# Kernel optimization log

Hardware: AMD Instinct MI355X
Metric: run time of the kernel (lower is better)

The kernel has to match this reference:

```python
import jax, jax.numpy as jnp
import numpy as np

BLOCK_SIZE = 1024
OUTLIER_SIGMA = 3.0
OUT_FEATURES = 11008
IN_FEATURES = 4096
TOKENS = 64


def _quantize_mixed_np(W):
    """Faithful numpy port of quantize_mixed (BLOCK_SIZE divides numel exactly here)."""
    flat = W.astype(np.float32).reshape(-1)
    nb = flat.size // BLOCK_SIZE
    blocks = flat.reshape(nb, BLOCK_SIZE)
    mu = blocks.mean(axis=1, keepdims=True)
    sig = np.maximum(blocks.std(axis=1, ddof=1, keepdims=True), 1e-8)  # torch.std is unbiased
    outlier = np.abs(blocks - mu) > OUTLIER_SIGMA * sig
    abs_max = np.maximum(np.abs(np.where(outlier, 0.0, blocks)).max(axis=1), 1e-8)
    scales = (abs_max / 127.0).astype(np.float16)
    q = np.clip(np.round(blocks / abs_max[:, None] * 127.0), -127, 127).astype(np.int8)
    all_pos = np.arange(nb, dtype=np.int64)[:, None] * BLOCK_SIZE + np.arange(BLOCK_SIZE, dtype=np.int64)[None, :]
    int8_data = q[~outlier]                      # row-major == torch order
    fp16_data = blocks[outlier].astype(np.float16)
    int8_pos = all_pos[~outlier].astype(np.int32)
    fp16_pos = all_pos[outlier].astype(np.int32)
    block_idx = np.nonzero(~outlier)[0].astype(np.int32)  # block index per int8 value
    return int8_data, fp16_data, scales, int8_pos, fp16_pos, block_idx


def setup_inputs() -> dict:
    key = jax.random.key(0)
    k_x, k_b = jax.random.split(key)
    rng = np.random.default_rng(0)
    W = (rng.standard_normal((OUT_FEATURES, IN_FEATURES)) * 0.02).astype(np.float32)
    int8_data, fp16_data, scales, int8_pos, fp16_pos, block_idx = _quantize_mixed_np(W)
    x = jax.random.normal(k_x, (TOKENS, IN_FEATURES), dtype=jnp.float16)
    bias = jax.random.normal(k_b, (OUT_FEATURES,), dtype=jnp.float16) * jnp.float16(0.02)
    return {
        "x": x,
        "int8_data": jnp.asarray(int8_data),
        "fp16_data": jnp.asarray(fp16_data),
        "scales": jnp.asarray(scales),
        "bias": bias,
        "int8_pos": jnp.asarray(int8_pos),
        "fp16_pos": jnp.asarray(fp16_pos),
        "block_idx": jnp.asarray(block_idx),
    }


def reference(x, int8_data, fp16_data, scales, bias, int8_pos, fp16_pos, block_idx):
    out_features = bias.shape[0]
    in_features = x.shape[1]
    numel = out_features * in_features  # divisible by BLOCK_SIZE for these dims
    # dequantize_mixed: scatter fp16 outliers and dequantized int8 values into flat fp16 buffer
    flat = jnp.zeros((numel,), dtype=jnp.float16)
    flat = flat.at[fp16_pos].set(fp16_data)
    flat = flat.at[int8_pos].set(int8_data.astype(jnp.float16) * scales[block_idx])
    W = flat.reshape(out_features, in_features)
    # F.linear(x, W, bias) in fp16
    return jnp.dot(x.astype(jnp.float16), W.T) + bias
```

## Files before the change

### kernel.cpp

```cpp
#include <hip/hip_runtime.h>
#include <hip/hip_fp16.h>

#define TOK   64
#define INF   4096
#define OUTF  11008
#define NSLC  (OUTF * INF / 64)
#define NBLK  (OUTF / 16)
#define KSPL  4

typedef __attribute__((ext_vector_type(8))) _Float16 half8;
typedef __attribute__((ext_vector_type(4))) _Float16 half4;
typedef __attribute__((ext_vector_type(4))) float floatx4;

__global__ __launch_bounds__(256) void precompute_kernel(
    const float* __restrict__ x, const int* __restrict__ fppos, int nf,
    _Float16* __restrict__ x16, int* __restrict__ cum64) {
  const int t = blockIdx.x * 256 + threadIdx.x;
  if (t < (TOK * INF) / 4) {
    const floatx4 f = *(const floatx4*)&x[t * 4];
    half4 h;
    h[0] = (_Float16)f[0]; h[1] = (_Float16)f[1];
    h[2] = (_Float16)f[2]; h[3] = (_Float16)f[3];
    *(half4*)&x16[t * 4] = h;
  }
  if (t <= NSLC) {
    const int target = t << 6;
    int lo = 0, hi = nf;
    while (lo < hi) {
      const int mid = (lo + hi) >> 1;
      if (fppos[mid] < target) lo = mid + 1; else hi = mid;
    }
    cum64[t] = lo;
  }
}

__global__ __launch_bounds__(256) void fused_gemm_kernel(
    const _Float16* __restrict__ x16, const int* __restrict__ i8,
    const float* __restrict__ fpdat, const int* __restrict__ fppos,
    const float* __restrict__ scales, const float* __restrict__ bias,
    const int* __restrict__ cum64, float* __restrict__ out, int n8) {
  __shared__ float red[4 * 64 * 16];

  const int tid  = threadIdx.x;
  const int wave = tid >> 6;
  const int lane = tid & 63;
  const int quad = lane >> 4;
  const int ln   = lane & 15;
  const int nt   = blockIdx.x >> 2;
  const int kq   = blockIdx.x & 3;
  const int n0   = nt * 16;

  const int r  = n0 + ln;
  const float s = scales[r * 4 + kq];
  const int kb = kq * 1024 + wave * 256 + quad * 8;
  const int pbase = r * INF + kb;

  const _Float16* ap = &x16[ln * INF + kb];

  floatx4 acc0 = {0,0,0,0}, acc1 = {0,0,0,0}, acc2 = {0,0,0,0}, acc3 = {0,0,0,0};

  int c0a[8], c1a[8];
#pragma unroll
  for (int st = 0; st < 8; ++st) {
    const int sI = (pbase + st * 32) >> 6;
    c0a[st] = cum64[sI];
    c1a[st] = cum64[sI + 1];
  }

#pragma unroll
  for (int st = 0; st < 8; ++st) {
    const int p  = pbase + st * 32;
    const int c0 = c0a[st], c1 = c1a[st];

    int f = 0, lt = 0;
    for (int j = c0; j < c1; ++j) {
      const int d = fppos[j] - p;
      lt += (d < 0);
      f |= ((unsigned)d < 8u) ? (1 << d) : 0;
    }

    const int i0 = p - c0 - lt;
    half8 bh;
    if ((f == 0) & (i0 + 8 <= n8)) {
      int l[8];
      __builtin_memcpy(l, &i8[i0], 32);
#pragma unroll
      for (int e = 0; e < 8; ++e) bh[e] = (_Float16)((float)l[e] * s);
    } else {
      int q = i0, jo = c0 + lt;
      const int m = n8 - 1;
#pragma unroll
      for (int e = 0; e < 8; ++e) {
        const int flg = (f >> e) & 1;
        float v;
        if (flg) { v = fpdat[jo]; ++jo; }
        else     { v = (float)i8[q > m ? m : q] * s; ++q; }
        bh[e] = (_Float16)v;
      }
    }

    const int ko = st * 32;
    const half8 a0 = *(const half8*)&ap[ko];
    const half8 a1 = *(const half8*)&ap[16 * INF + ko];
    const half8 a2 = *(const half8*)&ap[32 * INF + ko];
    const half8 a3 = *(const half8*)&ap[48 * INF + ko];
    acc0 = __builtin_amdgcn_mfma_f32_16x16x32_f16(a0, bh, acc0, 0, 0, 0);
    acc1 = __builtin_amdgcn_mfma_f32_16x16x32_f16(a1, bh, acc1, 0, 0, 0);
    acc2 = __builtin_amdgcn_mfma_f32_16x16x32_f16(a2, bh, acc2, 0, 0, 0);
    acc3 = __builtin_amdgcn_mfma_f32_16x16x32_f16(a3, bh, acc3, 0, 0, 0);
  }

  const int mb = quad * 4;
#pragma unroll
  for (int i = 0; i < 4; ++i) red[wave * 1024 + (mb + i)      * 16 + ln] = acc0[i];
#pragma unroll
  for (int i = 0; i < 4; ++i) red[wave * 1024 + (16 + mb + i) * 16 + ln] = acc1[i];
#pragma unroll
  for (int i = 0; i < 4; ++i) red[wave * 1024 + (32 + mb + i) * 16 + ln] = acc2[i];
#pragma unroll
  for (int i = 0; i < 4; ++i) red[wave * 1024 + (48 + mb + i) * 16 + ln] = acc3[i];
  __syncthreads();

#pragma unroll
  for (int c2 = 0; c2 < 4; ++c2) {
    const int cell = tid + c2 * 256;
    const int mm = cell >> 4, nn = cell & 15;
    float v = red[cell] + red[1024 + cell] + red[2048 + cell] + red[3072 + cell];
    if (kq == 0) v += bias[n0 + nn];
    atomicAdd(&out[mm * OUTF + n0 + nn], v);
  }
}

extern "C" void kernel_launch(void* const* d_in, const int* in_sizes, int n_in,
                              void* d_out, int out_size, void* d_ws,
                              size_t ws_size, hipStream_t stream) {
  const float* x      = (const float*)d_in[0];
  const int*   i8     = (const int*)d_in[1];
  const float* fpdat  = (const float*)d_in[2];
  const float* scales = (const float*)d_in[3];
  const float* bias   = (const float*)d_in[4];
  const int*   fppos  = (const int*)d_in[6];

  char* wsp = (char*)d_ws;
  _Float16* x16   = (_Float16*)wsp;
  int*      cum64 = (int*)(wsp + (size_t)TOK * INF * sizeof(_Float16));
  float*    out   = (float*)d_out;

  const int n8 = in_sizes[1];
  const int nf = in_sizes[2];

  hipMemsetAsync(out, 0, (size_t)out_size * sizeof(float), stream);
  precompute_kernel<<<(NSLC + 256) / 256 + 1, 256, 0, stream>>>(x, fppos, nf,
                                                                x16, cum64);
  fused_gemm_kernel<<<NBLK * KSPL, 256, 0, stream>>>(x16, i8, fpdat, fppos,
                                                     scales, bias, cum64, out,
                                                     n8);
}
```

Measured before the change: 488.9 us.

## Dequantize weight block into shared memory with coalesced int8 loads

The precompute step now builds a prefix-sum of outlier counts per 1024-element quantization block rather than per 64-element slice, which makes the precompute grid much smaller. The GEMM kernel first loads each row's outliers into shared memory. It then streams the int8 values for the whole block with coalesced vector loads, places each dequantized value at its shifted position in a padded shared-memory tile, and runs the MFMA loop from LDS. This replaces the per-thread scans over fppos and the scattered gathers inside the MFMA loop. The trade-offs are a per-element linear scan over up to 24 outlier keys, serial outlier handling by one thread per row, and outliers beyond 24 per block are silently dropped.

Result: no change. 486.5 us (-0.5%).

```diff
diff --git a/kernel.cpp b/kernel.cpp
--- a/kernel.cpp
+++ b/kernel.cpp
@@ -4,9 +4,11 @@
 #define TOK   64
 #define INF   4096
 #define OUTF  11008
-#define NSLC  (OUTF * INF / 64)
+#define NQB   44032
 #define NBLK  (OUTF / 16)
 #define KSPL  4
+#define BPAD  1032
+#define MAXO  24
 
 typedef __attribute__((ext_vector_type(8))) _Float16 half8;
 typedef __attribute__((ext_vector_type(4))) _Float16 half4;
@@ -14,7 +16,7 @@
 
 __global__ __launch_bounds__(256) void precompute_kernel(
     const float* __restrict__ x, const int* __restrict__ fppos, int nf,
-    _Float16* __restrict__ x16, int* __restrict__ cum64) {
+    _Float16* __restrict__ x16, int* __restrict__ cum) {
   const int t = blockIdx.x * 256 + threadIdx.x;
   if (t < (TOK * INF) / 4) {
     const floatx4 f = *(const floatx4*)&x[t * 4];
@@ -23,83 +25,110 @@
     h[2] = (_Float16)f[2]; h[3] = (_Float16)f[3];
     *(half4*)&x16[t * 4] = h;
   }
-  if (t <= NSLC) {
-    const int target = t << 6;
+  if (t <= NQB) {
+    const int target = t << 10;
     int lo = 0, hi = nf;
     while (lo < hi) {
       const int mid = (lo + hi) >> 1;
       if (fppos[mid] < target) lo = mid + 1; else hi = mid;
     }
-    cum64[t] = lo;
+    cum[t] = lo;
   }
 }
 
-__global__ __launch_bounds__(256) void fused_gemm_kernel(
+__global__ __launch_bounds__(256) void fused_kernel(
     const _Float16* __restrict__ x16, const int* __restrict__ i8,
     const float* __restrict__ fpdat, const int* __restrict__ fppos,
     const float* __restrict__ scales, const float* __restrict__ bias,
-    const int* __restrict__ cum64, float* __restrict__ out, int n8) {
-  __shared__ float red[4 * 64 * 16];
+    const int* __restrict__ cum, float* __restrict__ out, int n8) {
+  __shared__ __align__(16) _Float16 Bs[16 * BPAD];
+  __shared__ int   key_sh[16][MAXO];
+  __shared__ float oval_sh[16][MAXO];
 
-  const int tid  = threadIdx.x;
+  const int tid = threadIdx.x;
+  const int nt  = blockIdx.x >> 2;
+  const int kq  = blockIdx.x & 3;
+  const int n0  = nt * 16;
+
+  const int rr = tid >> 4;
+  const int jj = tid & 15;
+  const int r  = n0 + rr;
+  const int b  = r * 4 + kq;
+  const int T0 = cum[b], T1 = cum[b + 1];
+  const int nbout = T1 - T0;
+  const int nbo   = nbout < MAXO ? nbout : MAXO;
+  const int pos0  = r * INF + kq * 1024;
+  const int c_lo  = pos0 - T0;
+  const int nint  = 1024 - nbout;
+  const float s   = scales[b];
+
+  if (jj == 0) {
+    for (int i = 0; i < nbo; ++i) {
+      const int o = fppos[T0 + i] - pos0;
+      key_sh[rr][i] = o - i;
+      oval_sh[rr][i] = fpdat[T0 + i];
+    }
+  }
+  __syncthreads();
+
+  const int off  = c_lo & 3;
+  const int c_al = c_lo - off;
+#pragma unroll
+  for (int it = 0; it < 16; ++it) {
+    const int gi = c_al + 4 * (jj + 16 * it);
+    const int t0 = 4 * (jj + 16 * it) - off;
+    int l[4];
+    if (gi + 3 < n8) {
+      __builtin_memcpy(l, &i8[gi], 16);
+    } else {
+#pragma unroll
+      for (int e = 0; e < 4; ++e) {
+        int idx = gi + e; if (idx > n8 - 1) idx = n8 - 1;
+        l[e] = i8[idx];
+      }
+    }
+#pragma unroll
+    for (int e = 0; e < 4; ++e) {
+      const int t = t0 + e;
+      if ((unsigned)t < (unsigned)nint) {
+        int sft = 0;
+        for (int i = 0; i < nbo; ++i) sft += (key_sh[rr][i] <= t);
+        Bs[rr * BPAD + t + sft] = (_Float16)((float)l[e] * s);
+      }
+    }
+  }
+  if (off != 0 && jj == 0) {
+#pragma unroll
+    for (int e = 0; e < 4; ++e) {
+      const int t = 1024 - off + e;
+      if ((unsigned)t < (unsigned)nint) {
+        int idx = c_al + 1024 + e; if (idx > n8 - 1) idx = n8 - 1;
+        int sft = 0;
+        for (int i = 0; i < nbo; ++i) sft += (key_sh[rr][i] <= t);
+        Bs[rr * BPAD + t + sft] = (_Float16)((float)i8[idx] * s);
+      }
+    }
+  }
+  if (jj == 0) {
+    for (int i = 0; i < nbo; ++i)
+      Bs[rr * BPAD + key_sh[rr][i] + i] = (_Float16)oval_sh[rr][i];
+  }
+  __syncthreads();
+
   const int wave = tid >> 6;
   const int lane = tid & 63;
   const int quad = lane >> 4;
   const int ln   = lane & 15;
-  const int nt   = blockIdx.x >> 2;
-  const int kq   = blockIdx.x & 3;
-  const int n0   = nt * 16;
-
-  const int r  = n0 + ln;
-  const float s = scales[r * 4 + kq];
-  const int kb = kq * 1024 + wave * 256 + quad * 8;
-  const int pbase = r * INF + kb;
+  const int kb   = kq * 1024 + wave * 256 + quad * 8;
 
   const _Float16* ap = &x16[ln * INF + kb];
+  const _Float16* bp = &Bs[ln * BPAD + wave * 256 + quad * 8];
 
   floatx4 acc0 = {0,0,0,0}, acc1 = {0,0,0,0}, acc2 = {0,0,0,0}, acc3 = {0,0,0,0};
-
-  int c0a[8], c1a[8];
 #pragma unroll
   for (int st = 0; st < 8; ++st) {
-    const int sI = (pbase + st * 32) >> 6;
-    c0a[st] = cum64[sI];
-    c1a[st] = cum64[sI + 1];
-  }
-
-#pragma unroll
-  for (int st = 0; st < 8; ++st) {
-    const int p  = pbase + st * 32;
-    const int c0 = c0a[st], c1 = c1a[st];
-
-    int f = 0, lt = 0;
-    for (int j = c0; j < c1; ++j) {
-      const int d = fppos[j] - p;
-      lt += (d < 0);
-      f |= ((unsigned)d < 8u) ? (1 << d) : 0;
-    }
-
-    const int i0 = p - c0 - lt;
-    half8 bh;
-    if ((f == 0) & (i0 + 8 <= n8)) {
-      int l[8];
-      __builtin_memcpy(l, &i8[i0], 32);
-#pragma unroll
-      for (int e = 0; e < 8; ++e) bh[e] = (_Float16)((float)l[e] * s);
-    } else {
-      int q = i0, jo = c0 + lt;
-      const int m = n8 - 1;
-#pragma unroll
-      for (int e = 0; e < 8; ++e) {
-        const int flg = (f >> e) & 1;
-        float v;
-        if (flg) { v = fpdat[jo]; ++jo; }
-        else     { v = (float)i8[q > m ? m : q] * s; ++q; }
-        bh[e] = (_Float16)v;
-      }
-    }
-
     const int ko = st * 32;
+    const half8 bh = *(const half8*)&bp[ko];
     const half8 a0 = *(const half8*)&ap[ko];
     const half8 a1 = *(const half8*)&ap[16 * INF + ko];
     const half8 a2 = *(const half8*)&ap[32 * INF + ko];
@@ -109,7 +138,9 @@
     acc2 = __builtin_amdgcn_mfma_f32_16x16x32_f16(a2, bh, acc2, 0, 0, 0);
     acc3 = __builtin_amdgcn_mfma_f32_16x16x32_f16(a3, bh, acc3, 0, 0, 0);
   }
+  __syncthreads();
 
+  float* red = (float*)Bs;
   const int mb = quad * 4;
 #pragma unroll
   for (int i = 0; i < 4; ++i) red[wave * 1024 + (mb + i)      * 16 + ln] = acc0[i];
@@ -142,17 +173,15 @@
   const int*   fppos  = (const int*)d_in[6];
 
   char* wsp = (char*)d_ws;
-  _Float16* x16   = (_Float16*)wsp;
-  int*      cum64 = (int*)(wsp + (size_t)TOK * INF * sizeof(_Float16));
-  float*    out   = (float*)d_out;
+  _Float16* x16 = (_Float16*)wsp;
+  int*      cum = (int*)(wsp + (size_t)TOK * INF * sizeof(_Float16));
+  float*    out = (float*)d_out;
 
   const int n8 = in_sizes[1];
   const int nf = in_sizes[2];
 
   hipMemsetAsync(out, 0, (size_t)out_size * sizeof(float), stream);
-  precompute_kernel<<<(NSLC + 256) / 256 + 1, 256, 0, stream>>>(x, fppos, nf,
-                                                                x16, cum64);
-  fused_gemm_kernel<<<NBLK * KSPL, 256, 0, stream>>>(x16, i8, fpdat, fppos,
-                                                     scales, bias, cum64, out,
-                                                     n8);
+  precompute_kernel<<<256, 256, 0, stream>>>(x, fppos, nf, x16, cum);
+  fused_kernel<<<NBLK * KSPL, 256, 0, stream>>>(x16, i8, fpdat, fppos, scales,
+                                                bias, cum, out, n8);
 }
```

## Split fused dequant-GEMM into separate dequantization and GEMM kernels

Applied to the files above, without the earlier changes.

Moves dequantization out of the GEMM into a standalone kernel that writes a full fp16 weight matrix to workspace, then runs a plain MFMA GEMM reading it. This removes divergent outlier-scanning and irregular loads from the GEMM inner loop and gives the dequant pass contiguous per-thread work. In exchange it adds a large extra write and read of the materialized fp16 weights through global memory.

New measurement: 471.7 us. 1.04x faster.

```diff
diff --git a/kernel.cpp b/kernel.cpp
--- a/kernel.cpp
+++ b/kernel.cpp
@@ -4,13 +4,16 @@
 #define TOK   64
 #define INF   4096
 #define OUTF  11008
-#define NSLC  (OUTF * INF / 64)
+#define NUMEL (OUTF * INF)
+#define NSLC  (NUMEL / 64)
+#define NQB   (NUMEL / 1024)
 #define NBLK  (OUTF / 16)
 #define KSPL  4
 
 typedef __attribute__((ext_vector_type(8))) _Float16 half8;
 typedef __attribute__((ext_vector_type(4))) _Float16 half4;
 typedef __attribute__((ext_vector_type(4))) float floatx4;
+typedef __attribute__((ext_vector_type(4), aligned(4))) int int4u;
 
 __global__ __launch_bounds__(256) void precompute_kernel(
     const float* __restrict__ x, const int* __restrict__ fppos, int nf,
@@ -34,11 +37,95 @@
   }
 }
 
-__global__ __launch_bounds__(256) void fused_gemm_kernel(
-    const _Float16* __restrict__ x16, const int* __restrict__ i8,
-    const float* __restrict__ fpdat, const int* __restrict__ fppos,
-    const float* __restrict__ scales, const float* __restrict__ bias,
-    const int* __restrict__ cum64, float* __restrict__ out, int n8) {
+__global__ __launch_bounds__(256) void dequant_kernel(
+    const int* __restrict__ i8, const float* __restrict__ fpdat,
+    const int* __restrict__ fppos, const float* __restrict__ scales,
+    const int* __restrict__ cum64, _Float16* __restrict__ W, int n8) {
+  const int t   = blockIdx.x * 256 + threadIdx.x;
+  const int p0  = t * 8;
+  const int s64 = p0 >> 6;
+  const int c0  = cum64[s64];
+  const int c1  = cum64[s64 + 1];
+  const float s = scales[p0 >> 10];
+
+  int lt = 0, f = 0;
+  float ov[8];
+#pragma unroll
+  for (int e = 0; e < 8; ++e) ov[e] = 0.f;
+
+  const int w = c1 - c0;
+  if (w > 0) {
+    {
+      const int d = fppos[c0] - p0;
+      const float v = fpdat[c0];
+      lt += (d < 0);
+      if ((unsigned)d < 8u) {
+        f |= 1 << d;
+#pragma unroll
+        for (int e = 0; e < 8; ++e) ov[e] = (d == e) ? v : ov[e];
+      }
+    }
+    if (w > 1) {
+      const int d = fppos[c0 + 1] - p0;
+      const float v = fpdat[c0 + 1];
+      lt += (d < 0);
+      if ((unsigned)d < 8u) {
+        f |= 1 << d;
+#pragma unroll
+        for (int e = 0; e < 8; ++e) ov[e] = (d == e) ? v : ov[e];
+      }
+    }
+    for (int j = 2; j < w; ++j) {
+      const int d = fppos[c0 + j] - p0;
+      const float v = fpdat[c0 + j];
+      lt += (d < 0);
+      if ((unsigned)d < 8u) {
+        f |= 1 << d;
+#pragma unroll
+        for (int e = 0; e < 8; ++e) ov[e] = (d == e) ? v : ov[e];
+      }
+    }
+  }
+
+  const int i0 = p0 - c0 - lt;
+  half8 oh;
+  if (i0 + 8 <= n8) {
+    int l[8];
+    *(int4u*)&l[0] = *(const int4u*)&i8[i0];
+    *(int4u*)&l[4] = *(const int4u*)&i8[i0 + 4];
+    if (f == 0) {
+#pragma unroll
+      for (int e = 0; e < 8; ++e) oh[e] = (_Float16)((float)l[e] * s);
+    } else {
+      int q = 0;
+#pragma unroll
+      for (int e = 0; e < 8; ++e) {
+        const int flg = (f >> e) & 1;
+        int lv = l[0];
+#pragma unroll
+        for (int qq = 1; qq < 8; ++qq) lv = (q == qq) ? l[qq] : lv;
+        oh[e] = flg ? (_Float16)ov[e] : (_Float16)((float)lv * s);
+        q += 1 - flg;
+      }
+    }
+  } else {
+    int c = 0;
+    const int m = n8 - 1;
+#pragma unroll
+    for (int e = 0; e < 8; ++e) {
+      const int flg = (f >> e) & 1;
+      int idx = i0 + e - c;
+      idx = idx < 0 ? 0 : (idx > m ? m : idx);
+      oh[e] = flg ? (_Float16)ov[e] : (_Float16)((float)i8[idx] * s);
+      c += flg;
+    }
+  }
+  *(half8*)&W[p0] = oh;
+}
+
+__global__ __launch_bounds__(256) void gemm_kernel(
+    const _Float16* __restrict__ x16, const _Float16* __restrict__ W,
+    const float* __restrict__ bias, float* __restrict__ out) {
   __shared__ float red[4 * 64 * 16];
 
   const int tid  = threadIdx.x;
@@ -50,56 +137,15 @@
   const int kq   = blockIdx.x & 3;
   const int n0   = nt * 16;
 
-  const int r  = n0 + ln;
-  const float s = scales[r * 4 + kq];
   const int kb = kq * 1024 + wave * 256 + quad * 8;
-  const int pbase = r * INF + kb;
-
+  const _Float16* wp = &W[(n0 + ln) * INF + kb];
   const _Float16* ap = &x16[ln * INF + kb];
 
   floatx4 acc0 = {0,0,0,0}, acc1 = {0,0,0,0}, acc2 = {0,0,0,0}, acc3 = {0,0,0,0};
-
-  int c0a[8], c1a[8];
 #pragma unroll
   for (int st = 0; st < 8; ++st) {
-    const int sI = (pbase + st * 32) >> 6;
-    c0a[st] = cum64[sI];
-    c1a[st] = cum64[sI + 1];
-  }
-
-#pragma unroll
-  for (int st = 0; st < 8; ++st) {
-    const int p  = pbase + st * 32;
-    const int c0 = c0a[st], c1 = c1a[st];
-
-    int f = 0, lt = 0;
-    for (int j = c0; j < c1; ++j) {
-      const int d = fppos[j] - p;
-      lt += (d < 0);
-      f |= ((unsigned)d < 8u) ? (1 << d) : 0;
-    }
-
-    const int i0 = p - c0 - lt;
-    half8 bh;
-    if ((f == 0) & (i0 + 8 <= n8)) {
-      int l[8];
-      __builtin_memcpy(l, &i8[i0], 32);
-#pragma unroll
-      for (int e = 0; e < 8; ++e) bh[e] = (_Float16)((float)l[e] * s);
-    } else {
-      int q = i0, jo = c0 + lt;
-      const int m = n8 - 1;
-#pragma unroll
-      for (int e = 0; e < 8; ++e) {
-        const int flg = (f >> e) & 1;
-        float v;
-        if (flg) { v = fpdat[jo]; ++jo; }
-        else     { v = (float)i8[q > m ? m : q] * s; ++q; }
-        bh[e] = (_Float16)v;
-      }
-    }
-
     const int ko = st * 32;
+    const half8 bh = *(const half8*)&wp[ko];
     const half8 a0 = *(const half8*)&ap[ko];
     const half8 a1 = *(const half8*)&ap[16 * INF + ko];
     const half8 a2 = *(const half8*)&ap[32 * INF + ko];
@@ -142,8 +188,10 @@
   const int*   fppos  = (const int*)d_in[6];
 
   char* wsp = (char*)d_ws;
-  _Float16* x16   = (_Float16*)wsp;
-  int*      cum64 = (int*)(wsp + (size_t)TOK * INF * sizeof(_Float16));
+  _Float16* W     = (_Float16*)wsp;
+  _Float16* x16   = (_Float16*)(wsp + (size_t)NUMEL * sizeof(_Float16));
+  int*      cum64 = (int*)(wsp + (size_t)NUMEL * sizeof(_Float16)
+                               + (size_t)TOK * INF * sizeof(_Float16));
   float*    out   = (float*)d_out;
 
   const int n8 = in_sizes[1];
@@ -152,7 +200,7 @@
   hipMemsetAsync(out, 0, (size_t)out_size * sizeof(float), stream);
   precompute_kernel<<<(NSLC + 256) / 256 + 1, 256, 0, stream>>>(x, fppos, nf,
                                                                 x16, cum64);
-  fused_gemm_kernel<<<NBLK * KSPL, 256, 0, stream>>>(x16, i8, fpdat, fppos,
-                                                     scales, bias, cum64, out,
-                                                     n8);
-}
+  dequant_kernel<<<NUMEL / (8 * 256), 256, 0, stream>>>(i8, fpdat, fppos,
+                                                        scales, cum64, W, n8);
+  gemm_kernel<<<NBLK * KSPL, 256, 0, stream>>>(x16, W, bias, out);
+}
```
